# Performance work log

Hardware: AMD Instinct MI355X
Metric: run time of the kernel (lower is better)

The kernel has to match this reference:

```python
import jax, jax.numpy as jnp
import numpy as np

DIM, HEADS, DH, CHUNK, DEPTH = 1024, 8, 128, 64, 2
BATCH, SEQLEN = 2, 4096
MAX_LR = 0.01
EPS = 1e-6


def _rmsnorm(x, g=None):
    y = x * jax.lax.rsqrt(jnp.mean(x * x, axis=-1, keepdims=True) + EPS)
    return y * g if g is not None else y


def _mem_mlp(ws, x):
    # MemoryMLP: x @ W0, then silu before each subsequent layer
    x = x @ ws[0]
    for w in ws[1:]:
        x = jax.nn.silu(x) @ w
    return x


def _assoc_scan(gates, x):
    # y_t = gates_t * y_{t-1} + x_t along axis 3 (chunk axis)
    g = jnp.broadcast_to(gates, x.shape)
    def op(a, b):
        ga, xa = a
        gb, xb = b
        return ga * gb, gb * xa + xb
    _, y = jax.lax.associative_scan(op, (g, x), axis=3)
    return y


def setup_inputs() -> dict:
    key = jax.random.key(0)
    ks = jax.random.split(key, 12)
    b, n, d, h, dh = BATCH, SEQLEN, DIM, HEADS, DH
    di = h * dh
    lin = lambda k, i, o: jax.random.normal(k, (i, o), jnp.float32) * np.float32(1.0 / np.sqrt(i))
    return {
        "seq": jax.random.normal(ks[0], (b, n, d), jnp.float32),
        "store_norm_g": jnp.ones((d,), jnp.float32),
        "retrieve_norm_g": jnp.ones((d,), jnp.float32),
        "w_kv": lin(ks[1], d, 2 * di),
        "w_q": lin(ks[2], d, di),
        "w_step": lin(ks[3], d, h),
        "w_mom": lin(ks[4], d, h),
        "w_decay": lin(ks[5], d, h),
        "w_gate": lin(ks[6], d, h),
        "w_combine": lin(ks[7], di, d),
        "mh_gamma": jnp.zeros((h, 1, dh), jnp.float32),
        "mem_w0": lin(ks[8], dh, dh),
        "mem_w1": lin(ks[9], dh, dh),
    }


def reference(seq, store_norm_g, retrieve_norm_g, w_kv, w_q, w_step, w_mom,
              w_decay, w_gate, w_combine, mh_gamma, mem_w0, mem_w1):
    b, n, d = seq.shape
    h, dh, c = HEADS, DH, CHUNK
    nc = n // c
    mem_ws = (mem_w0, mem_w1)

    # ---------------- store memories (chunked test-time training) ----------------
    ss = _rmsnorm(seq, store_norm_g)                                    # (b,n,d)
    lr = jax.nn.sigmoid(jnp.einsum('bnd,dh->bhn', ss, w_step)) * MAX_LR  # adaptive step
    lr = lr.reshape(b, h, nc, c)
    cmean = ss.reshape(b, nc, c, d).mean(axis=2)                        # chunk mean-reduce
    mom_gate = jax.nn.sigmoid(jnp.einsum('bnd,dh->bhn', cmean, w_mom))   # (b,h,nc)
    decay = jax.nn.sigmoid(jnp.einsum('bnd,dh->bhn', cmean, w_decay))    # (b,h,nc)

    kv = ss @ w_kv                                                      # (b,n,2*h*dh)
    keys, values = jnp.split(kv, 2, axis=-1)
    split = lambda t: t.reshape(b, n, h, dh).transpose(0, 2, 1, 3).reshape(b, h, nc, c, dh)
    keys, values = split(keys), split(values)

    # per-chunk grad of weighted mse wrt memory MLP weights (vmap(grad), as in torch.func)
    def chunk_loss(ws, k, lrc, v):
        pred = _mem_mlp(ws, k)                                          # (c,dh)
        return jnp.sum(jnp.mean((pred - v) ** 2, axis=-1) * lrc)
    flat = lambda t: t.reshape(b * h * nc, c, dh)
    grads = jax.vmap(jax.grad(chunk_loss), in_axes=(None, 0, 0, 0))(
        mem_ws, flat(keys), lr.reshape(b * h * nc, c), flat(values))
    grads = jnp.stack([g.reshape(b, h, nc, dh, dh) for g in grads])     # (depth,b,h,nc,dh,dh)
    surprise = -grads

    gm = mom_gate[None, :, :, :, None, None]
    gd = (1.0 - decay)[None, :, :, :, None, None]
    momentum = _assoc_scan(gm, surprise)                                # momentum scan over chunks
    updates = _assoc_scan(gd, momentum)                                 # decayed cumulative weight deltas

    # ---------------- retrieve memories ----------------
    sr = _rmsnorm(seq, retrieve_norm_g)
    sr = jnp.pad(sr[:, c - 1:], ((0, 0), (0, c - 1), (0, 0)))           # causal shift by chunk-1
    q = (sr @ w_q).reshape(b, n, h, dh).transpose(0, 2, 1, 3).reshape(b, h, nc, c, dh)

    w0 = mem_w0 + updates[0]                                            # (b,h,nc,dh,dh)
    w1 = mem_w1 + updates[1]
    x = jnp.einsum('bhncd,bhnde->bhnce', q, w0)
    vals = jnp.einsum('bhncd,bhnde->bhnce', jax.nn.silu(x), w1)         # (b,h,nc,c,dh)
    vals = vals.reshape(b, h, n, dh)

    vals = _rmsnorm(vals) * (mh_gamma + 1.0)                            # multihead rmsnorm
    gate = jax.nn.sigmoid(jnp.einsum('bnd,dh->bhn', sr, w_gate))[..., None]
    vals = vals * gate                                                  # retrieve gate (heads>1)
    vals = vals.transpose(0, 2, 1, 3).reshape(b, n, h * dh)             # merge heads
    out = vals @ w_combine                                              # combine heads
    out = jnp.pad(out, ((0, 0), (c - 1, 0), (0, 0)))[:, :n]             # restore alignment
    return out
```

## Files before the change

### kernel.cpp

```cpp
#include <hip/hip_runtime.h>
#include <stdint.h>


#define SEQ 4096
#define NTOK 8192

typedef unsigned short u16;
typedef __attribute__((ext_vector_type(8))) short short8;
typedef __attribute__((ext_vector_type(4))) float f32x4;
typedef __attribute__((ext_vector_type(2))) unsigned int u32x2;

__device__ __forceinline__ u16 f2b(float f) {
  union { float f; uint32_t u; } c; c.f = f;
  uint32_t u = c.u;
  uint32_t r = (u + 0x7fffu + ((u >> 16) & 1u)) >> 16;
  return (u16)r;
}
__device__ __forceinline__ float b2f(u16 h) {
  union { uint32_t u; float f; } c; c.u = ((uint32_t)h) << 16;
  return c.f;
}
__device__ __forceinline__ float sigm(float x) { return 1.f / (1.f + __expf(-x)); }
__device__ __forceinline__ uint32_t pk2(float a, float b) {
  return (uint32_t)f2b(a) | ((uint32_t)f2b(b) << 16);
}
__device__ __forceinline__ void gl16(const void* g, void* l) {
  __builtin_amdgcn_global_load_lds(
      (const __attribute__((address_space(1))) unsigned int*)g,
      (__attribute__((address_space(3))) unsigned int*)l, 16, 0, 0);
}

__device__ __forceinline__ int sidx(int r, int c) {
  return r*128 + ((((c>>3) ^ (r&7))<<3) | (c&7));
}
__device__ __forceinline__ short8 frag_row_lds128(const u16* buf, int row, int ks, int l4) {
  int g = ks*4 + l4;
  return *(const short8*)&buf[row*128 + ((g ^ (row&7))<<3)];
}
__device__ __forceinline__ short8 frag_tile(const u16* t, int row, int ks, int l4) {
  return *(const short8*)&t[row*64 + (((ks*4 + l4) ^ (row&7))<<3)];
}
__device__ __forceinline__ int taddr(int c, int r0) {
  return c*64 + (r0 ^ ((c&7)<<3));
}


__global__ __launch_bounds__(256) void transpose_bf16(
    const float* __restrict__ src, u16* __restrict__ dst, int R, int C)
{
  __shared__ u16 tile[64*66];
  int tiles_x = C >> 6;
  int tx = blockIdx.x % tiles_x, ty = blockIdx.x / tiles_x;
  int c0 = tx*64, r0 = ty*64;
#pragma unroll
  for (int it=0; it<16; ++it) {
    int idx = it*256 + threadIdx.x;
    int rr = idx>>6, cc = idx&63;
    tile[cc*66 + rr] = f2b(src[(size_t)(r0+rr)*C + c0+cc]);
  }
  __syncthreads();
#pragma unroll
  for (int it=0; it<16; ++it) {
    int idx = it*256 + threadIdx.x;
    int rr = idx>>6, cc = idx&63;
    dst[(size_t)(c0+rr)*R + r0+cc] = tile[rr*66 + cc];
  }
}

__global__ __launch_bounds__(256) void smallprep(
    const float* __restrict__ w0, const float* __restrict__ w1,
    u16* __restrict__ w0Ts, u16* __restrict__ w1Ts, u16* __restrict__ w1bs)
{
  int id = blockIdx.x*256 + threadIdx.x;
  int i = id>>7, j = id&127;
  float a = w0[id], b = w1[id];
  w0Ts[sidx(j,i)] = f2b(a);
  w1Ts[sidx(j,i)] = f2b(b);
  w1bs[sidx(i,j)] = f2b(b);
}


__global__ __launch_bounds__(256) void norms_kernel(
    const float* __restrict__ seq, const float* __restrict__ gs,
    const float* __restrict__ gr, const float* __restrict__ wstep,
    const float* __restrict__ wgate, u16* __restrict__ ss,
    u16* __restrict__ sr, float* __restrict__ lr, float* __restrict__ gate)
{
  int t = blockIdx.x; int b = t>>12, pos = t&4095;
  int tid = threadIdx.x;
  const float* row = seq + (size_t)t*1024;
  float x[4]; float ssq = 0.f;
#pragma unroll
  for (int i=0;i<4;++i){ x[i]=row[i*256+tid]; ssq += x[i]*x[i]; }
  for (int m=32;m;m>>=1) ssq += __shfl_xor(ssq, m);
  __shared__ float red[4];
  __shared__ float r2[4][16];
  int wv = tid>>6;
  if ((tid&63)==0) red[wv] = ssq;
  __syncthreads();
  float tot = red[0]+red[1]+red[2]+red[3];
  float inv = rsqrtf(tot*(1.f/1024.f) + 1e-6f);
  float ps[8], pg[8];
#pragma unroll
  for (int h=0;h<8;++h){ ps[h]=0.f; pg[h]=0.f; }
#pragma unroll
  for (int i=0;i<4;++i) {
    int d = i*256+tid;
    float sv = x[i]*inv*gs[d];
    float rv = x[i]*inv*gr[d];
    ss[(size_t)t*1024+d] = f2b(sv);
    sr[(size_t)t*1024+d] = f2b(rv);
#pragma unroll
    for (int h=0;h<8;++h) { ps[h] += sv*wstep[d*8+h]; pg[h] += rv*wgate[d*8+h]; }
  }
#pragma unroll
  for (int h=0;h<8;++h)
    for (int m=32;m;m>>=1){ ps[h] += __shfl_xor(ps[h],m); pg[h] += __shfl_xor(pg[h],m); }
  if ((tid&63)==0) {
#pragma unroll
    for (int h=0;h<8;++h){ r2[wv][h]=ps[h]; r2[wv][8+h]=pg[h]; }
  }
  __syncthreads();
  if (tid < 16) {
    float s = r2[0][tid]+r2[1][tid]+r2[2][tid]+r2[3][tid];
    float sg = sigm(s);
    if (tid<8) lr[((size_t)(b*8+tid))*4096 + pos] = sg*0.01f;
    else gate[((size_t)(b*8+(tid-8)))*4096 + pos] = sg;
  }
}


__global__ __launch_bounds__(256) void chunkgates_kernel(
    const u16* __restrict__ ss, const float* __restrict__ wmom,
    const float* __restrict__ wdec, float* __restrict__ mg,
    float* __restrict__ d1m)
{
  int bc = blockIdx.x; int b = bc>>6, ch = bc&63;
  size_t t0 = (size_t)(b*4096 + ch*64)*1024;
  int tid = threadIdx.x;
  float cm[4]; cm[0]=cm[1]=cm[2]=cm[3]=0.f;
  for (int tok=0; tok<64; ++tok) {
#pragma unroll
    for (int i=0;i<4;++i)
      cm[i] += b2f(ss[t0 + (size_t)tok*1024 + i*256 + tid]);
  }
  float pm[8], pd[8];
#pragma unroll
  for (int h=0;h<8;++h){ pm[h]=0.f; pd[h]=0.f; }
#pragma unroll
  for (int i=0;i<4;++i) {
    float v = cm[i]*(1.f/64.f);
    int d = i*256+tid;
#pragma unroll
    for (int h=0;h<8;++h){ pm[h]+=v*wmom[d*8+h]; pd[h]+=v*wdec[d*8+h]; }
  }
#pragma unroll
  for (int h=0;h<8;++h)
    for (int m=32;m;m>>=1){ pm[h] += __shfl_xor(pm[h],m); pd[h] += __shfl_xor(pd[h],m); }
  __shared__ float r2[4][16];
  int wv = tid>>6;
  if ((tid&63)==0) {
#pragma unroll
    for (int h=0;h<8;++h){ r2[wv][h]=pm[h]; r2[wv][8+h]=pd[h]; }
  }
  __syncthreads();
  if (tid < 16) {
    float s = r2[0][tid]+r2[1][tid]+r2[2][tid]+r2[3][tid];
    if (tid<8) mg[(b*8+tid)*64 + ch] = sigm(s);
    else d1m[(b*8+(tid-8))*64 + ch] = 1.f - sigm(s);
  }
}


__global__ __launch_bounds__(256) void gemm_bt(
    const u16* __restrict__ A, const u16* __restrict__ Bt,
    void* __restrict__ C, int M, int N, int K, int out_f32,
    u16* __restrict__ kvT)
{
  __shared__ __align__(16) u16 As[128*64];
  __shared__ __align__(16) u16 Bs[128*64];
  int tid = threadIdx.x;
  int wv = tid>>6, lane = tid&63;
  int wr = wv>>1, wc = wv&1;
  int l15 = lane&15, l4 = lane>>4;
  int rl = lane>>3;
  int cg = (lane&7) ^ rl;
  int nwg = gridDim.x*gridDim.y;
  int wg  = blockIdx.y*gridDim.x + blockIdx.x;
  int cpx = nwg >> 3;
  int swz = (wg & 7)*cpx + (wg >> 3);
  int bx = swz % gridDim.x, by = swz / gridDim.x;
  int brow = by*128, bcol = bx*128;
  f32x4 acc[4][4] = {};
  for (int kt=0; kt<K; kt+=64) {
#pragma unroll
    for (int it=0; it<4; ++it) {
      int rw0 = it*32 + wv*8;
      gl16(&A[(size_t)(brow+rw0+rl)*K + kt + cg*8], &As[rw0*64]);
      gl16(&Bt[(size_t)(bcol+rw0+rl)*K + kt + cg*8], &Bs[rw0*64]);
    }
    __syncthreads();
#pragma unroll
    for (int ks=0; ks<2; ++ks) {
      short8 af[4], bfr[4];
#pragma unroll
      for (int m=0;m<4;++m) {
        int row = wr*64 + m*16 + l15;
        int g = ks*4 + l4;
        af[m] = *(const short8*)&As[row*64 + ((g ^ (row&7))<<3)];
      }
#pragma unroll
      for (int n=0;n<4;++n) {
        int row = wc*64 + n*16 + l15;
        int g = ks*4 + l4;
        bfr[n] = *(const short8*)&Bs[row*64 + ((g ^ (row&7))<<3)];
      }
#pragma unroll
      for (int m=0;m<4;++m)
#pragma unroll
        for (int n=0;n<4;++n)
          acc[m][n] = __builtin_amdgcn_mfma_f32_16x16x32_bf16(af[m], bfr[n], acc[m][n], 0,0,0);
    }
    __syncthreads();
  }
#pragma unroll
  for (int m=0;m<4;++m) {
#pragma unroll
    for (int n=0;n<4;++n) {
      int col = bcol + wc*64 + n*16 + l15;
#pragma unroll
      for (int j=0;j<4;++j) {
        int row = brow + wr*64 + m*16 + l4*4 + j;
        if (out_f32) ((float*)C)[(size_t)row*N + col] = acc[m][n][j];
        else ((u16*)C)[(size_t)row*N + col] = f2b(acc[m][n][j]);
      }
    }
  }
  if (kvT) {
#pragma unroll
    for (int m=0;m<4;++m) {
#pragma unroll
      for (int n=0;n<4;++n) {
        int col = bcol + wc*64 + n*16 + l15;
        if (col < 1024) {
          int row0 = brow + wr*64 + m*16 + l4*4;
          int d = col & 127;
          int chunk = ((row0>>12)*8 + (col>>7))*64 + ((row0&4095)>>6);
          int rr = row0 & 63;
          u32x2 p; p[0] = pk2(acc[m][n][0], acc[m][n][1]);
                   p[1] = pk2(acc[m][n][2], acc[m][n][3]);
          *(u32x2*)&kvT[(size_t)chunk*8192 + taddr(d, rr)] = p;
        }
      }
    }
  }
}


__global__ __launch_bounds__(512) void mlp_fwd(
    const u16* __restrict__ kvout, const float* __restrict__ lr,
    const u16* __restrict__ w0Ts, const u16* __restrict__ w1Ts,
    const u16* __restrict__ w1bs,
    u16* __restrict__ aTg, u16* __restrict__ dpTg, u16* __restrict__ dxTg)
{
  __shared__ __align__(16) u16 W0L[16384];
  __shared__ __align__(16) u16 W1L[16384];
  __shared__ __align__(16) u16 WBL[16384];
  __shared__ __align__(16) u16 abuf[16384];
  int tid = threadIdx.x;
  int w = tid>>6, lane = tid&63;
  int l15 = lane&15, l4 = lane>>4;
#pragma unroll
  for (int it=0; it<4; ++it) {
    int wb = it*512 + w*64;
    gl16((const short8*)w0Ts + wb + lane, (short8*)W0L + wb);
    gl16((const short8*)w1Ts + wb + lane, (short8*)W1L + wb);
    gl16((const short8*)w1bs + wb + lane, (short8*)WBL + wb);
  }
  __syncthreads();
  u16* ab = abuf + w*2048;
  int r0 = l4*4;
  int q = w&3, half = w>>2;
  int rb = q*16;
#pragma unroll
  for (int it2=0; it2<2; ++it2) {
    int cidx = blockIdx.x*4 + it2*2 + half;
    int bh = cidx>>6, ch = cidx&63;
    int b = bh>>3, hh = bh&7;
    size_t t0 = (size_t)(b*4096 + ch*64 + rb);
    size_t tout = (size_t)cidx*8192;
    f32x4 lrv = *(const f32x4*)&lr[(size_t)bh*4096 + ch*64 + rb + r0];

    f32x4 x1[8] = {};
#pragma unroll
    for (int ks=0; ks<4; ++ks) {
      short8 af = *(const short8*)&kvout[(t0 + l15)*2048 + hh*128 + ks*32 + l4*8];
#pragma unroll
      for (int n=0;n<8;++n) {
        short8 bf = frag_row_lds128(W0L, n*16+l15, ks, l4);
        x1[n] = __builtin_amdgcn_mfma_f32_16x16x32_bf16(af, bf, x1[n], 0,0,0);
      }
    }
#pragma unroll
    for (int n=0;n<8;++n) {
      int c = n*16 + l15;
      float av[4];
#pragma unroll
      for (int j=0;j<4;++j){ float xv = x1[n][j]; av[j] = xv*sigm(xv); }
      ab[sidx(r0+0,c)] = f2b(av[0]);
      ab[sidx(r0+1,c)] = f2b(av[1]);
      ab[sidx(r0+2,c)] = f2b(av[2]);
      ab[sidx(r0+3,c)] = f2b(av[3]);
      u32x2 p; p[0] = pk2(av[0],av[1]); p[1] = pk2(av[2],av[3]);
      *(u32x2*)&aTg[tout + taddr(c, rb + r0)] = p;
    }
    f32x4 pr[8] = {};
#pragma unroll
    for (int ks=0; ks<4; ++ks) {
      short8 af = frag_row_lds128(ab, l15, ks, l4);
#pragma unroll
      for (int n=0;n<8;++n) {
        short8 bf = frag_row_lds128(W1L, n*16+l15, ks, l4);
        pr[n] = __builtin_amdgcn_mfma_f32_16x16x32_bf16(af, bf, pr[n], 0,0,0);
      }
    }
#pragma unroll
    for (int n=0;n<8;++n) {
      int c = n*16 + l15;
      float dv[4];
#pragma unroll
      for (int j=0;j<4;++j) {
        float vv = b2f(kvout[(t0+r0+j)*2048 + 1024 + hh*128 + c]);
        dv[j] = 0.015625f * lrv[j] * (pr[n][j] - vv);
      }
      ab[sidx(r0+0,c)] = f2b(dv[0]);
      ab[sidx(r0+1,c)] = f2b(dv[1]);
      ab[sidx(r0+2,c)] = f2b(dv[2]);
      ab[sidx(r0+3,c)] = f2b(dv[3]);
      u32x2 p; p[0] = pk2(dv[0],dv[1]); p[1] = pk2(dv[2],dv[3]);
      *(u32x2*)&dpTg[tout + taddr(c, rb + r0)] = p;
    }
    f32x4 da[8] = {};
#pragma unroll
    for (int ks=0; ks<4; ++ks) {
      short8 af = frag_row_lds128(ab, l15, ks, l4);
#pragma unroll
      for (int n=0;n<8;++n) {
        short8 bf = frag_row_lds128(WBL, n*16+l15, ks, l4);
        da[n] = __builtin_amdgcn_mfma_f32_16x16x32_bf16(af, bf, da[n], 0,0,0);
      }
    }
#pragma unroll
    for (int n=0;n<8;++n) {
      int c = n*16 + l15;
      float d[4];
#pragma unroll
      for (int j=0;j<4;++j) {
        float xv = x1[n][j];
        float sg = sigm(xv);
        d[j] = da[n][j]*(sg*(1.f + xv*(1.f - sg)));
      }
      u32x2 p; p[0] = pk2(d[0],d[1]); p[1] = pk2(d[2],d[3]);
      *(u32x2*)&dxTg[tout + taddr(c, rb + r0)] = p;
    }
  }
}


__global__ __launch_bounds__(256) void grad_op(
    const u16* __restrict__ dpT, const u16* __restrict__ aT,
    const u16* __restrict__ dxT, const u16* __restrict__ kT,
    u16* __restrict__ S)
{
  __shared__ __align__(16) u16 lds[16384];
  int bid = blockIdx.x;
  int op = bid >> 10;
  int sub = bid & 1023, bh = sub>>6, ch = sub&63;
  size_t tin = (size_t)sub*8192;
  const u16* Ain = op ? (dxT + tin) : (dpT + tin);
  const u16* Bin = op ? (kT  + tin) : (aT  + tin);
  int tid = threadIdx.x;
  int w = tid>>6, lane = tid&63;
  int l15 = lane&15, l4 = lane>>4;

#pragma unroll
  for (int it=0; it<4; ++it) {
    int wb = it*256 + w*64;
    gl16((const short8*)Ain + wb + lane, (short8*)lds + wb);
    gl16((const short8*)Bin + wb + lane, (short8*)(lds+8192) + wb);
  }
  __syncthreads();

  f32x4 g[2][8] = {};
#pragma unroll
  for (int ks=0; ks<2; ++ks) {
    short8 af[2];
#pragma unroll
    for (int mi=0; mi<2; ++mi)
      af[mi] = frag_tile(lds, w*32 + mi*16 + l15, ks, l4);
#pragma unroll
    for (int n=0;n<8;++n) {
      short8 bf = frag_tile(lds+8192, n*16 + l15, ks, l4);
#pragma unroll
      for (int mi=0;mi<2;++mi)
        g[mi][n] = __builtin_amdgcn_mfma_f32_16x16x32_bf16(af[mi], bf, g[mi][n], 0,0,0);
    }
  }
  __syncthreads();

#pragma unroll
  for (int mi=0;mi<2;++mi)
#pragma unroll
    for (int n=0;n<8;++n)
#pragma unroll
      for (int j=0;j<4;++j) {
        int m = w*32 + mi*16 + l4*4 + j, c = n*16 + l15;
        lds[sidx(m,c)] = f2b(-g[mi][n][j]);
      }
  __syncthreads();

  u16* Sout = S + ((size_t)((op ? bh : 16+bh))*64 + ch)*16384;
#pragma unroll
  for (int it=0; it<8; ++it)
    ((short8*)Sout)[it*256+tid] = ((const short8*)lds)[it*256+tid];
}


__global__ __launch_bounds__(256) void scan_kernel(
    u16* __restrict__ S, const float* __restrict__ mg, const float* __restrict__ d1m,
    const u16* __restrict__ w0Ts, const u16* __restrict__ w1Ts)
{
  int bidx = blockIdx.x;
  int eblk = bidx & 63;
  int mbh = bidx >> 6;
  int bh = mbh & 15;
  int e = eblk*256 + threadIdx.x;
  u16* base = S + (size_t)mbh*64*16384 + e;
  float wv = b2f(((mbh < 16) ? w0Ts : w1Ts)[e]);
  const float* g1 = mg + bh*64;
  const float* g2 = d1m + bh*64;
  float mom = 0.f, upd = 0.f;
  for (int c2=0; c2<64; ++c2) {
    float s = b2f(base[(size_t)c2*16384]);
    mom = g1[c2]*mom + s;
    upd = g2[c2]*upd + mom;
    base[(size_t)c2*16384] = f2b(wv + upd);
  }
}


__global__ __launch_bounds__(256) void retrieve_kernel(
    const u16* __restrict__ qn, const u16* __restrict__ W,
    const float* __restrict__ gamma, const float* __restrict__ gate,
    u16* __restrict__ vals)
{
  __shared__ __align__(16) u16 W0s[16384];
  __shared__ __align__(16) u16 W1s[16384];
  __shared__ __align__(16) u16 QA[8192];
  int bid = blockIdx.x;
  int bh = bid>>6, ch = bid&63;
  int b = bh>>3, h = bh&7;
  int tid = threadIdx.x;
  int w = tid>>6, lane = tid&63;
  int l15 = lane&15, l4 = lane>>4;
  const u16* W0g = W + ((size_t)bh*64 + ch)*16384;
  const u16* W1g = W + ((size_t)(16+bh)*64 + ch)*16384;
#pragma unroll
  for (int it=0; it<8; ++it) {
    int wb = it*256 + w*64;
    gl16((const short8*)W0g + wb + lane, (short8*)W0s + wb);
    gl16((const short8*)W1g + wb + lane, (short8*)W1s + wb);
  }
  u16* qa = QA + w*2048;
#pragma unroll
  for (int it=0; it<4; ++it) {
    int task = it*64 + lane;
    int rloc = task>>4, g = task&15;
    int posn = ch*64 + w*16 + rloc + 63;
    short8 v;
    if (posn < 4096) v = *(const short8*)&qn[((size_t)(b*4096+posn))*1024 + h*128 + g*8];
    else {
#pragma unroll
      for (int i=0;i<8;++i) v[i]=0;
    }
    *(short8*)&qa[rloc*128 + ((g ^ (rloc&7))<<3)] = v;
  }
  __syncthreads();
  f32x4 xx[8] = {};
#pragma unroll
  for (int ks=0; ks<4; ++ks) {
    short8 af = frag_row_lds128(qa, l15, ks, l4);
#pragma unroll
    for (int n=0;n<8;++n) {
      short8 bf = frag_row_lds128(W0s, n*16+l15, ks, l4);
      xx[n] = __builtin_amdgcn_mfma_f32_16x16x32_bf16(af, bf, xx[n], 0,0,0);
    }
  }
  int r0 = l4*4;
#pragma unroll
  for (int n=0;n<8;++n) {
    int c = n*16 + l15;
#pragma unroll
    for (int j=0;j<4;++j) {
      float xv = xx[n][j];
      qa[sidx(r0+j,c)] = f2b(xv * sigm(xv));
    }
  }
  f32x4 vv[8] = {};
#pragma unroll
  for (int ks=0; ks<4; ++ks) {
    short8 af = frag_row_lds128(qa, l15, ks, l4);
#pragma unroll
    for (int n=0;n<8;++n) {
      short8 bf = frag_row_lds128(W1s, n*16+l15, ks, l4);
      vv[n] = __builtin_amdgcn_mfma_f32_16x16x32_bf16(af, bf, vv[n], 0,0,0);
    }
  }
#pragma unroll
  for (int j=0;j<4;++j) {
    float ssq = 0.f;
#pragma unroll
    for (int n=0;n<8;++n) ssq += vv[n][j]*vv[n][j];
    ssq += __shfl_xor(ssq,1); ssq += __shfl_xor(ssq,2);
    ssq += __shfl_xor(ssq,4); ssq += __shfl_xor(ssq,8);
    float rms = rsqrtf(ssq*(1.f/128.f) + 1e-6f);
    int posn = ch*64 + w*16 + r0 + j + 63;
    if (posn < 4096) {
      float gt = gate[(size_t)bh*4096 + posn];
      size_t orow = ((size_t)(b*4096+posn))*1024 + h*128;
#pragma unroll
      for (int n=0;n<8;++n) {
        int c = n*16 + l15;
        vals[orow + c] = f2b(vv[n][j]*rms*(1.f + gamma[h*128+c])*gt);
      }
    }
  }
}

extern "C" void kernel_launch(void* const* d_in, const int* in_sizes, int n_in,
                              void* d_out, int out_size, void* d_ws, size_t ws_size,
                              hipStream_t stream) {
  const float* seq    = (const float*)d_in[0];
  const float* gstore = (const float*)d_in[1];
  const float* gret   = (const float*)d_in[2];
  const float* wkv    = (const float*)d_in[3];
  const float* wq     = (const float*)d_in[4];
  const float* wstep  = (const float*)d_in[5];
  const float* wmom   = (const float*)d_in[6];
  const float* wdec   = (const float*)d_in[7];
  const float* wgate  = (const float*)d_in[8];
  const float* wcomb  = (const float*)d_in[9];
  const float* gamma  = (const float*)d_in[10];
  const float* w0f    = (const float*)d_in[11];
  const float* w1f    = (const float*)d_in[12];
  float* out = (float*)d_out;
  (void)in_sizes; (void)n_in; (void)out_size; (void)ws_size;

  char* p = (char*)d_ws;
  size_t off = 0;
  auto alloc = [&](size_t bytes) -> void* {
    void* r = p + off; off += (bytes + 255) & ~(size_t)255; return r;
  };
  u16* wkvT   = (u16*)alloc((size_t)2048*1024*2);
  u16* wqT    = (u16*)alloc((size_t)1024*1024*2);
  u16* wcombT = (u16*)alloc((size_t)1024*1024*2);
  u16* w0Ts   = (u16*)alloc(16384*2);
  u16* w1Ts   = (u16*)alloc(16384*2);
  u16* w1bs   = (u16*)alloc(16384*2);
  u16* ss     = (u16*)alloc((size_t)NTOK*1024*2);
  u16* sr     = (u16*)alloc((size_t)NTOK*1024*2);
  u16* kvout  = (u16*)alloc((size_t)NTOK*2048*2);
  u16* qn     = (u16*)alloc((size_t)NTOK*1024*2);
  u16* vals   = (u16*)alloc((size_t)NTOK*1024*2);
  float* lr   = (float*)alloc((size_t)16*4096*4);
  float* gate = (float*)alloc((size_t)16*4096*4);
  float* mg   = (float*)alloc(1024*4);
  float* d1m  = (float*)alloc(1024*4);
  u16* S      = (u16*)alloc((size_t)32*64*16384*2);
  u16* kTg    = (u16*)alloc((size_t)1024*8192*2);
  u16* aTg    = (u16*)alloc((size_t)1024*8192*2);
  u16* dpTg   = (u16*)alloc((size_t)1024*8192*2);
  u16* dxTg   = (u16*)alloc((size_t)1024*8192*2);

  transpose_bf16<<<dim3(512),dim3(256),0,stream>>>(wkv, wkvT, 1024, 2048);
  transpose_bf16<<<dim3(256),dim3(256),0,stream>>>(wq, wqT, 1024, 1024);
  transpose_bf16<<<dim3(256),dim3(256),0,stream>>>(wcomb, wcombT, 1024, 1024);
  smallprep<<<dim3(64),dim3(256),0,stream>>>(w0f, w1f, w0Ts, w1Ts, w1bs);
  norms_kernel<<<dim3(NTOK),dim3(256),0,stream>>>(seq, gstore, gret, wstep, wgate, ss, sr, lr, gate);
  chunkgates_kernel<<<dim3(128),dim3(256),0,stream>>>(ss, wmom, wdec, mg, d1m);
  gemm_bt<<<dim3(16,64),dim3(256),0,stream>>>(ss, wkvT, kvout, 8192, 2048, 1024, 0, kTg);
  gemm_bt<<<dim3(8,64),dim3(256),0,stream>>>(sr, wqT, qn, 8192, 1024, 1024, 0, nullptr);
  mlp_fwd<<<dim3(256),dim3(512),0,stream>>>(kvout, lr, w0Ts, w1Ts, w1bs, aTg, dpTg, dxTg);
  grad_op<<<dim3(2048),dim3(256),0,stream>>>(dpTg, aTg, dxTg, kTg, S);
  scan_kernel<<<dim3(2048),dim3(256),0,stream>>>(S, mg, d1m, w0Ts, w1Ts);
  hipMemsetAsync(vals, 0, 63*1024*2, stream);
  hipMemsetAsync(vals + (size_t)4096*1024, 0, 63*1024*2, stream);
  retrieve_kernel<<<dim3(1024),dim3(256),0,stream>>>(qn, S, gamma, gate, vals);
  gemm_bt<<<dim3(8,64),dim3(256),0,stream>>>(vals, wcombT, out, 8192, 1024, 1024, 1, nullptr);
}
```

Before: 273.4 us.

## Double-buffer GEMM LDS tiles and use 8 waves per block

```diff
diff --git a/kernel.cpp b/kernel.cpp
--- a/kernel.cpp
+++ b/kernel.cpp
@@ -172,16 +172,16 @@
 }
 
 
-__global__ __launch_bounds__(256) void gemm_bt(
+__global__ __launch_bounds__(512, 4) void gemm_bt(
     const u16* __restrict__ A, const u16* __restrict__ Bt,
     void* __restrict__ C, int M, int N, int K, int out_f32,
     u16* __restrict__ kvT)
 {
-  __shared__ __align__(16) u16 As[128*64];
-  __shared__ __align__(16) u16 Bs[128*64];
+  __shared__ __align__(16) u16 As[2][128*64];
+  __shared__ __align__(16) u16 Bs[2][128*64];
   int tid = threadIdx.x;
-  int wv = tid>>6, lane = tid&63;
-  int wr = wv>>1, wc = wv&1;
+  int w = tid>>6, lane = tid&63;
+  int wr = w>>2, wc = w&3;
   int l15 = lane&15, l4 = lane>>4;
   int rl = lane>>3;
   int cg = (lane&7) ^ rl;
@@ -191,43 +191,53 @@
   int swz = (wg & 7)*cpx + (wg >> 3);
   int bx = swz % gridDim.x, by = swz / gridDim.x;
   int brow = by*128, bcol = bx*128;
-  f32x4 acc[4][4] = {};
-  for (int kt=0; kt<K; kt+=64) {
-#pragma unroll
-    for (int it=0; it<4; ++it) {
-      int rw0 = it*32 + wv*8;
-      gl16(&A[(size_t)(brow+rw0+rl)*K + kt + cg*8], &As[rw0*64]);
-      gl16(&Bt[(size_t)(bcol+rw0+rl)*K + kt + cg*8], &Bs[rw0*64]);
-    }
-    __syncthreads();
+  f32x4 acc[4][2] = {};
+
+  auto STAGE = [&](int buf, int kt) {
+#pragma unroll
+    for (int i=0;i<2;++i) {
+      int row = w*16 + i*8;
+      gl16(&A [(size_t)(brow+row+rl)*K + kt + cg*8], &As[buf][row*64]);
+      gl16(&Bt[(size_t)(bcol+row+rl)*K + kt + cg*8], &Bs[buf][row*64]);
+    }
+  };
+
+  int nk = K >> 6;
+  STAGE(0, 0);
+  asm volatile("s_waitcnt vmcnt(0)");
+  __syncthreads();
+  for (int t=0; t<nk; ++t) {
+    int cur = t & 1;
+    if (t+1 < nk) STAGE(cur^1, (t+1)*64);
 #pragma unroll
     for (int ks=0; ks<2; ++ks) {
-      short8 af[4], bfr[4];
+      short8 af[4], bf[2];
 #pragma unroll
       for (int m=0;m<4;++m) {
         int row = wr*64 + m*16 + l15;
         int g = ks*4 + l4;
-        af[m] = *(const short8*)&As[row*64 + ((g ^ (row&7))<<3)];
-      }
-#pragma unroll
-      for (int n=0;n<4;++n) {
-        int row = wc*64 + n*16 + l15;
+        af[m] = *(const short8*)&As[cur][row*64 + ((g ^ (row&7))<<3)];
+      }
+#pragma unroll
+      for (int n=0;n<2;++n) {
+        int row = wc*32 + n*16 + l15;
         int g = ks*4 + l4;
-        bfr[n] = *(const short8*)&Bs[row*64 + ((g ^ (row&7))<<3)];
+        bf[n] = *(const short8*)&Bs[cur][row*64 + ((g ^ (row&7))<<3)];
       }
 #pragma unroll
       for (int m=0;m<4;++m)
 #pragma unroll
-        for (int n=0;n<4;++n)
-          acc[m][n] = __builtin_amdgcn_mfma_f32_16x16x32_bf16(af[m], bfr[n], acc[m][n], 0,0,0);
-    }
+        for (int n=0;n<2;++n)
+          acc[m][n] = __builtin_amdgcn_mfma_f32_16x16x32_bf16(af[m], bf[n], acc[m][n], 0,0,0);
+    }
+    asm volatile("s_waitcnt vmcnt(0)");
     __syncthreads();
   }
 #pragma unroll
   for (int m=0;m<4;++m) {
 #pragma unroll
-    for (int n=0;n<4;++n) {
-      int col = bcol + wc*64 + n*16 + l15;
+    for (int n=0;n<2;++n) {
+      int col = bcol + wc*32 + n*16 + l15;
 #pragma unroll
       for (int j=0;j<4;++j) {
         int row = brow + wr*64 + m*16 + l4*4 + j;
@@ -240,8 +250,8 @@
 #pragma unroll
     for (int m=0;m<4;++m) {
 #pragma unroll
-      for (int n=0;n<4;++n) {
-        int col = bcol + wc*64 + n*16 + l15;
+      for (int n=0;n<2;++n) {
+        int col = bcol + wc*32 + n*16 + l15;
         if (col < 1024) {
           int row0 = brow + wr*64 + m*16 + l4*4;
           int d = col & 127;
@@ -588,13 +598,13 @@
   smallprep<<<dim3(64),dim3(256),0,stream>>>(w0f, w1f, w0Ts, w1Ts, w1bs);
   norms_kernel<<<dim3(NTOK),dim3(256),0,stream>>>(seq, gstore, gret, wstep, wgate, ss, sr, lr, gate);
   chunkgates_kernel<<<dim3(128),dim3(256),0,stream>>>(ss, wmom, wdec, mg, d1m);
-  gemm_bt<<<dim3(16,64),dim3(256),0,stream>>>(ss, wkvT, kvout, 8192, 2048, 1024, 0, kTg);
-  gemm_bt<<<dim3(8,64),dim3(256),0,stream>>>(sr, wqT, qn, 8192, 1024, 1024, 0, nullptr);
+  gemm_bt<<<dim3(16,64),dim3(512),0,stream>>>(ss, wkvT, kvout, 8192, 2048, 1024, 0, kTg);
+  gemm_bt<<<dim3(8,64),dim3(512),0,stream>>>(sr, wqT, qn, 8192, 1024, 1024, 0, nullptr);
   mlp_fwd<<<dim3(256),dim3(512),0,stream>>>(kvout, lr, w0Ts, w1Ts, w1bs, aTg, dpTg, dxTg);
   grad_op<<<dim3(2048),dim3(256),0,stream>>>(dpTg, aTg, dxTg, kTg, S);
   scan_kernel<<<dim3(2048),dim3(256),0,stream>>>(S, mg, d1m, w0Ts, w1Ts);
   hipMemsetAsync(vals, 0, 63*1024*2, stream);
   hipMemsetAsync(vals + (size_t)4096*1024, 0, 63*1024*2, stream);
   retrieve_kernel<<<dim3(1024),dim3(256),0,stream>>>(qn, S, gamma, gate, vals);
-  gemm_bt<<<dim3(8,64),dim3(256),0,stream>>>(vals, wcombT, out, 8192, 1024, 1024, 1, nullptr);
-}
+  gemm_bt<<<dim3(8,64),dim3(512),0,stream>>>(vals, wcombT, out, 8192, 1024, 1024, 1, nullptr);
+}
```

Result: faster. 259.0 us (-5.3%).
